# Kernel optimization log

Measured on AMD Instinct MI355X. Metric: run time of the kernel, lower is better.

The kernel has to match this reference:

```python
import jax, jax.numpy as jnp
import numpy as np

BITS = 4
GROUP = 128
M, K, N = 16, 4096, 11008


def setup_inputs() -> dict:
    key = jax.random.key(0)
    k1, k2, k3 = jax.random.split(key, 3)
    A = jax.random.normal(k1, (M, K), dtype=jnp.float16)
    # packed 4-bit weights: 2 nibbles per byte, stored as int32 holding 0..255
    qweight = jax.random.randint(k2, (N, K * BITS // 8), 0, 256, dtype=jnp.int32)
    # small positive-ish scales like real GPTQ checkpoints
    scales = (jax.random.normal(k3, (N, K // GROUP)) * 0.01 + 0.02).astype(jnp.float16)
    zeros = jnp.zeros((N, K // GROUP), dtype=jnp.float16)
    bias = jnp.zeros((N,), dtype=jnp.float16)
    return {"A": A, "qweight": qweight, "scales": scales, "zeros": zeros, "bias": bias}


def _dequant(qweight, scales, zeros):
    # qweight: (N, K//2) packed; element idx -> byte idx//2, low nibble if idx even
    low = qweight & 0xF
    high = (qweight >> 4) & 0xF
    w_int = jnp.stack([low, high], axis=-1).reshape(qweight.shape[0], -1)  # (N, K)
    # per-group dequant with 'original' zeros: W = (q - z) * s
    s = jnp.repeat(scales, GROUP, axis=1)  # (N, K)
    z = jnp.repeat(zeros, GROUP, axis=1)   # (N, K)
    return (w_int.astype(jnp.float16) - z) * s


def reference(A, qweight, scales, zeros, bias):
    W = _dequant(qweight, scales, zeros)           # (N, K) fp16
    return jnp.matmul(A, W.T) + bias               # (M, N) fp16
```

## Files before the change

### kernel.cpp

```cpp
#include <hip/hip_runtime.h>

#define KK 4096
#define NN 11008
#define GRP 128
#define KW (KK / 2)
#define NGRP (KK / GRP)

using short8  = __attribute__((ext_vector_type(8))) short;
using float4v = __attribute__((ext_vector_type(4))) float;

static __device__ __forceinline__ unsigned int pack_bf16(float lo, float hi) {
    unsigned int ul = __builtin_bit_cast(unsigned int, lo);
    unsigned int uh = __builtin_bit_cast(unsigned int, hi);
    ul = (ul + 0x7FFFu + ((ul >> 16) & 1u)) >> 16;
    uh = (uh + 0x7FFFu + ((uh >> 16) & 1u)) & 0xFFFF0000u;
    return ul | uh;
}
static __device__ __forceinline__ float bf16val(float f) {
    unsigned int u = __builtin_bit_cast(unsigned int, f);
    u = (u + 0x7FFFu + ((u >> 16) & 1u)) & 0xFFFF0000u;
    return __builtin_bit_cast(float, u);
}

#define WS_RS_OFF 131072

__global__ __launch_bounds__(256) void prep_kernel(
    const float* __restrict__ A, unsigned short* __restrict__ wsA,
    float* __restrict__ rowsum)
{
    const int b = blockIdx.x;
    if (b < 32) {
        const int idx = (b * 256 + threadIdx.x) * 8;
        float4v x0 = *(const float4v*)(A + idx);
        float4v x1 = *(const float4v*)(A + idx + 4);
        union { short8 s8; unsigned int u[4]; } p;
        p.u[0] = pack_bf16(x0[0], x0[1]);
        p.u[1] = pack_bf16(x0[2], x0[3]);
        p.u[2] = pack_bf16(x1[0], x1[1]);
        p.u[3] = pack_bf16(x1[2], x1[3]);
        *(short8*)(wsA + idx) = p.s8;
    } else {
        const int sid = (b - 32) * 16 + (threadIdx.x >> 4);
        const int m = sid >> 5, g = sid & 31;
        const int j = threadIdx.x & 15;
        const float* p = A + (size_t)m * KK + g * GRP + j * 8;
        float4v x0 = *(const float4v*)p;
        float4v x1 = *(const float4v*)(p + 4);
        float sum = bf16val(x0[0]) + bf16val(x0[1]) + bf16val(x0[2]) + bf16val(x0[3])
                  + bf16val(x1[0]) + bf16val(x1[1]) + bf16val(x1[2]) + bf16val(x1[3]);
        sum += __shfl_xor(sum, 1, 16);
        sum += __shfl_xor(sum, 2, 16);
        sum += __shfl_xor(sum, 4, 16);
        sum += __shfl_xor(sum, 8, 16);
        if (j == 0) rowsum[sid] = sum;
    }
}

__global__ __launch_bounds__(256) void qgemm_kernel(
    const int*   __restrict__ qweight,
    const float* __restrict__ scales,
    const float* __restrict__ zeros,
    const float* __restrict__ bias,
    const unsigned short* __restrict__ wsA,
    const float* __restrict__ rowsum,
    float*       __restrict__ out)
{
    const int nt = blockIdx.x >> 1;
    const int kh = blockIdx.x & 1;
    const int n0 = nt * 16;
    const int wid  = threadIdx.x >> 6;
    const int lane = threadIdx.x & 63;
    const int nl   = lane & 15;
    const int quad = lane >> 4;
    const int n    = n0 + nl;

    const int kbase = kh * 2048 + wid * 512;
    const int g0    = kbase >> 7;

    const int*            qrow = qweight + (size_t)n * KW;
    const unsigned short* arow = wsA + (size_t)nl * KK;

    int4   wb[2][4];
    short8 ab[2][4];

    #pragma unroll
    for (int t = 0; t < 4; ++t) {
        const int k0 = kbase + t * 32 + quad * 8;
        wb[0][t] = *(const int4*)(qrow + (k0 >> 1));
        ab[0][t] = *(const short8*)(arow + k0);
    }
    float s_cur = scales[n * NGRP + g0];

    float4v acc = {0.f, 0.f, 0.f, 0.f};

    #pragma unroll
    for (int g = 0; g < 4; ++g) {
        const int cur = g & 1, nxt = cur ^ 1;
        float s_nxt = 0.f;
        if (g < 3) {
            #pragma unroll
            for (int t = 0; t < 4; ++t) {
                const int k0 = kbase + (g + 1) * GRP + t * 32 + quad * 8;
                wb[nxt][t] = *(const int4*)(qrow + (k0 >> 1));
                ab[nxt][t] = *(const short8*)(arow + k0);
            }
            s_nxt = scales[n * NGRP + g0 + g + 1];
        }

        float4v accg = {0.f, 0.f, 0.f, 0.f};
        #pragma unroll
        for (int t = 0; t < 4; ++t) {
            const unsigned int w0 = (unsigned int)wb[cur][t].x;
            const unsigned int w1 = (unsigned int)wb[cur][t].y;
            const unsigned int w2 = (unsigned int)wb[cur][t].z;
            const unsigned int w3 = (unsigned int)wb[cur][t].w;
            union { short8 s8; unsigned int u[4]; } bf;
            bf.u[0] = (w0 & 0xFu) | ((w0 << 12) & 0x000F0000u) | 0x43004300u;
            bf.u[1] = (w1 & 0xFu) | ((w1 << 12) & 0x000F0000u) | 0x43004300u;
            bf.u[2] = (w2 & 0xFu) | ((w2 << 12) & 0x000F0000u) | 0x43004300u;
            bf.u[3] = (w3 & 0xFu) | ((w3 << 12) & 0x000F0000u) | 0x43004300u;
            accg = __builtin_amdgcn_mfma_f32_16x16x32_bf16(ab[cur][t], bf.s8, accg, 0, 0, 0);
        }
        #pragma unroll
        for (int r = 0; r < 4; ++r)
            acc[r] = __builtin_fmaf(s_cur, accg[r], acc[r]);
        s_cur = s_nxt;
    }

    __shared__ float red[4][16][16];
    #pragma unroll
    for (int r = 0; r < 4; ++r)
        red[wid][quad * 4 + r][nl] = acc[r];
    __syncthreads();

    const int t  = threadIdx.x;
    const int m  = t >> 4;
    const int nn = t & 15;
    const int ng = n0 + nn;
    float val = red[0][m][nn] + red[1][m][nn] + red[2][m][nn] + red[3][m][nn];

    const int gh0 = kh * 16;
    const float* srow = scales + (size_t)ng * NGRP + gh0;
    const float* zrow = zeros  + (size_t)ng * NGRP + gh0;
    const float* rsm  = rowsum + m * NGRP + gh0;
    float corr = 0.f;
    #pragma unroll
    for (int gg = 0; gg < 16; ++gg)
        corr = __builtin_fmaf(srow[gg] * (128.0f + zrow[gg]), rsm[gg], corr);
    val -= corr;
    if (kh == 0) val += bias[ng];
    atomicAdd(&out[(size_t)m * NN + ng], val);
}

extern "C" void kernel_launch(void* const* d_in, const int* in_sizes, int n_in,
                              void* d_out, int out_size, void* d_ws, size_t ws_size,
                              hipStream_t stream) {
    const float* A       = (const float*)d_in[0];
    const int*   qweight = (const int*)d_in[1];
    const float* scales  = (const float*)d_in[2];
    const float* zeros   = (const float*)d_in[3];
    const float* bias    = (const float*)d_in[4];
    float*       out     = (float*)d_out;

    unsigned short* wsA = (unsigned short*)d_ws;
    float* rowsum       = (float*)((char*)d_ws + WS_RS_OFF);

    prep_kernel<<<dim3(64), dim3(256), 0, stream>>>(A, wsA, rowsum);
    qgemm_kernel<<<dim3(2 * NN / 16), dim3(256), 0, stream>>>(
        qweight, scales, zeros, bias, wsA, rowsum, out);
}
```

Measured before the change: 153.7 us.

## Stage packed weight rows through padded LDS with coalesced row-contiguous loads

Weight bytes for the 16-row tile are now loaded cooperatively, with each half-wave reading 512 contiguous bytes of one row. They are staged through double-buffered, padded shared memory before each wave reads its MFMA fragments from there. Each wave now covers interleaved 32-wide k slices within every 128-group instead of its own 512-wide k range. The goal is better DRAM coalescing than the earlier per-lane strided 16-byte row loads. In exchange it adds a __syncthreads per stage, reduces register prefetch depth, and issues one MFMA per scale group instead of four.

```diff
diff --git a/kernel.cpp b/kernel.cpp
--- a/kernel.cpp
+++ b/kernel.cpp
@@ -2,9 +2,12 @@
 
 #define KK 4096
 #define NN 11008
-#define GRP 128
+#define NGRP 32
 #define KW (KK / 2)
-#define NGRP (KK / GRP)
+#define ROWB 8192
+#define LROW 528
+#define TILEB (16 * LROW)
+#define WS_RS_OFF 131072
 
 using short8  = __attribute__((ext_vector_type(8))) short;
 using float4v = __attribute__((ext_vector_type(4))) float;
@@ -21,8 +24,6 @@
     u = (u + 0x7FFFu + ((u >> 16) & 1u)) & 0xFFFF0000u;
     return __builtin_bit_cast(float, u);
 }
-
-#define WS_RS_OFF 131072
 
 __global__ __launch_bounds__(256) void prep_kernel(
     const float* __restrict__ A, unsigned short* __restrict__ wsA,
@@ -43,7 +44,7 @@
         const int sid = (b - 32) * 16 + (threadIdx.x >> 4);
         const int m = sid >> 5, g = sid & 31;
         const int j = threadIdx.x & 15;
-        const float* p = A + (size_t)m * KK + g * GRP + j * 8;
+        const float* p = A + (size_t)m * KK + g * 128 + j * 8;
         float4v x0 = *(const float4v*)p;
         float4v x1 = *(const float4v*)(p + 4);
         float sum = bf16val(x0[0]) + bf16val(x0[1]) + bf16val(x0[2]) + bf16val(x0[3])
@@ -72,59 +73,55 @@
     const int lane = threadIdx.x & 63;
     const int nl   = lane & 15;
     const int quad = lane >> 4;
-    const int n    = n0 + nl;
 
-    const int kbase = kh * 2048 + wid * 512;
-    const int g0    = kbase >> 7;
+    __shared__ __align__(16) char lds[2 * TILEB];
 
-    const int*            qrow = qweight + (size_t)n * KW;
+    const char* qbase = (const char*)qweight + (size_t)n0 * ROWB + kh * 4096;
+    const int   r0    = wid * 4 + (lane >> 5);
+    const int   sbyte = (lane & 31) * 16;
+    const char* gp0 = qbase + (size_t)r0 * ROWB + sbyte;
+    const char* gp1 = qbase + (size_t)(r0 + 2) * ROWB + sbyte;
+    char* lw0 = lds + r0 * LROW + sbyte;
+    char* lw1 = lds + (r0 + 2) * LROW + sbyte;
+
     const unsigned short* arow = wsA + (size_t)nl * KK;
+    const float*          srow = scales + (size_t)(n0 + nl) * NGRP + kh * 16;
+    const char*           fr   = lds + nl * LROW + wid * 64 + quad * 16;
 
-    int4   wb[2][4];
-    short8 ab[2][4];
-
-    #pragma unroll
-    for (int t = 0; t < 4; ++t) {
-        const int k0 = kbase + t * 32 + quad * 8;
-        wb[0][t] = *(const int4*)(qrow + (k0 >> 1));
-        ab[0][t] = *(const short8*)(arow + k0);
-    }
-    float s_cur = scales[n * NGRP + g0];
+    int4 ra = *(const int4*)(gp0);
+    int4 rb = *(const int4*)(gp1);
 
     float4v acc = {0.f, 0.f, 0.f, 0.f};
 
-    #pragma unroll
-    for (int g = 0; g < 4; ++g) {
-        const int cur = g & 1, nxt = cur ^ 1;
-        float s_nxt = 0.f;
-        if (g < 3) {
-            #pragma unroll
-            for (int t = 0; t < 4; ++t) {
-                const int k0 = kbase + (g + 1) * GRP + t * 32 + quad * 8;
-                wb[nxt][t] = *(const int4*)(qrow + (k0 >> 1));
-                ab[nxt][t] = *(const short8*)(arow + k0);
-            }
-            s_nxt = scales[n * NGRP + g0 + g + 1];
+    for (int s = 0; s < 8; ++s) {
+        const int bo = (s & 1) * TILEB;
+        *(int4*)(lw0 + bo) = ra;
+        *(int4*)(lw1 + bo) = rb;
+        if (s < 7) {
+            ra = *(const int4*)(gp0 + (s + 1) * 512);
+            rb = *(const int4*)(gp1 + (s + 1) * 512);
         }
+        __syncthreads();
 
-        float4v accg = {0.f, 0.f, 0.f, 0.f};
         #pragma unroll
-        for (int t = 0; t < 4; ++t) {
-            const unsigned int w0 = (unsigned int)wb[cur][t].x;
-            const unsigned int w1 = (unsigned int)wb[cur][t].y;
-            const unsigned int w2 = (unsigned int)wb[cur][t].z;
-            const unsigned int w3 = (unsigned int)wb[cur][t].w;
+        for (int gg = 0; gg < 2; ++gg) {
+            const int k0 = kh * 2048 + (s * 2 + gg) * 128 + wid * 32 + quad * 8;
+            short8 a = *(const short8*)(arow + k0);
+            int4 wv = *(const int4*)(fr + bo + gg * 256);
             union { short8 s8; unsigned int u[4]; } bf;
+            const unsigned int w0 = (unsigned int)wv.x, w1 = (unsigned int)wv.y;
+            const unsigned int w2 = (unsigned int)wv.z, w3 = (unsigned int)wv.w;
             bf.u[0] = (w0 & 0xFu) | ((w0 << 12) & 0x000F0000u) | 0x43004300u;
             bf.u[1] = (w1 & 0xFu) | ((w1 << 12) & 0x000F0000u) | 0x43004300u;
             bf.u[2] = (w2 & 0xFu) | ((w2 << 12) & 0x000F0000u) | 0x43004300u;
             bf.u[3] = (w3 & 0xFu) | ((w3 << 12) & 0x000F0000u) | 0x43004300u;
-            accg = __builtin_amdgcn_mfma_f32_16x16x32_bf16(ab[cur][t], bf.s8, accg, 0, 0, 0);
+            float4v z4 = {0.f, 0.f, 0.f, 0.f};
+            float4v accg = __builtin_amdgcn_mfma_f32_16x16x32_bf16(a, bf.s8, z4, 0, 0, 0);
+            const float sg = srow[s * 2 + gg];
+            #pragma unroll
+            for (int r = 0; r < 4; ++r)
+                acc[r] = __builtin_fmaf(sg, accg[r], acc[r]);
         }
-        #pragma unroll
-        for (int r = 0; r < 4; ++r)
-            acc[r] = __builtin_fmaf(s_cur, accg[r], acc[r]);
-        s_cur = s_nxt;
     }
 
     __shared__ float red[4][16][16];
@@ -140,13 +137,13 @@
     float val = red[0][m][nn] + red[1][m][nn] + red[2][m][nn] + red[3][m][nn];
 
     const int gh0 = kh * 16;
-    const float* srow = scales + (size_t)ng * NGRP + gh0;
-    const float* zrow = zeros  + (size_t)ng * NGRP + gh0;
-    const float* rsm  = rowsum + m * NGRP + gh0;
+    const float* sr  = scales + (size_t)ng * NGRP + gh0;
+    const float* zr  = zeros  + (size_t)ng * NGRP + gh0;
+    const float* rsm = rowsum + m * NGRP + gh0;
     float corr = 0.f;
     #pragma unroll
     for (int gg = 0; gg < 16; ++gg)
-        corr = __builtin_fmaf(srow[gg] * (128.0f + zrow[gg]), rsm[gg], corr);
+        corr = __builtin_fmaf(sr[gg] * (128.0f + zr[gg]), rsm[gg], corr);
     val -= corr;
     if (kh == 0) val += bias[ng];
     atomicAdd(&out[(size_t)m * NN + ng], val);
```

New measurement: 151.0 us. Within noise of the previous version (-1.7%).
